# Performance work log

Measured on AMD Instinct MI355X. Metric: run time of the kernel, lower is better.

The kernel has to match this reference:

```python
import jax, jax.numpy as jnp
import numpy as np

N_ITERS = 5

def setup_inputs() -> dict:
    key = jax.random.key(0)
    k_in, k_ind, k_w = jax.random.split(key, 3)
    inputs = jax.random.normal(k_in, (2, 256, 256, 1), dtype=jnp.float32)
    # indices must be valid for spatial dims [256,256] (iter 1) and [217,721] (iters 2-5)
    ind1 = jax.random.randint(k_ind, (367, 217, 721, 2), 0, 217, dtype=jnp.int32)
    w1 = jax.random.uniform(k_w, (367, 217, 721, 1, 1), dtype=jnp.float32)
    lambda1 = jnp.asarray(0.1, dtype=jnp.float32)
    return {"inputs": inputs, "ind1": ind1, "w1": w1, "lambda1": lambda1}


def reference(inputs, ind1, w1, lambda1):
    # inputs: [B,H,W,C]; ind1: [367,217,721,2]; w1: [367,217,721,1,1]; lambda1: scalar
    i0 = ind1[..., 0]  # [367,217,721] -> indexes dim0 of [H,W,C,B]
    i1 = ind1[..., 1]  # [367,217,721] -> indexes dim1
    y = inputs
    for _ in range(N_ITERS):
        yt = jnp.transpose(y, (1, 2, 3, 0))          # [H,W,C,B]
        gathered = yt[i0, i1]                        # [367,217,721,C,B] (gather_nd)
        y = jnp.sum(gathered * w1, axis=0)           # [217,721,C,B]
        y = jnp.transpose(y, (3, 0, 1, 2))           # [B,217,721,C]
        y = lambda1 * y
    return y
```

## Files before the change

### kernel.cpp

```cpp
#include <hip/hip_runtime.h>
#include <hip/hip_fp16.h>
#include <stdint.h>

#define K_    367
#define P_    217
#define Q_    721
#define QC    217
#define CPQ   (QC*QC)
#define CPQV  47092
#define TPQ   109368
#define YSTR  47104
#define PQ_   (P_*Q_)
#define TOT   ((long long)K_*PQ_)
#define NC    ((long long)K_*CPQ)
#define NTAIL ((long long)K_*TPQ)
#define SL    (NTAIL/8)
#define NVC   (CPQV/4)
#define NVT   (TPQ/4)
#define NPAD  (3*K_)
#define LDSH  47092

__device__ __forceinline__ uint32_t encode_entry(int i0, int i1, float wv) {
    uint32_t idx2 = ((uint32_t)(i0 * QC + i1)) << 1;
    uint32_t hb = (uint32_t)__half_as_ushort(__float2half(wv));
    return idx2 | (hb << 17);
}

#define GATHER(X, ACC) { uint32_t x_ = (X); \
    float g_ = __half2float(*(const __half*)((const char*)ylds + (x_ & 0x1FFFEu))); \
    float w_ = __half2float(__ushort_as_half((unsigned short)(x_ >> 17))); \
    ACC = fmaf(w_, g_, ACC); }

#define FILL_LDS() { \
    const float4* s4_ = (const float4*)yplane; \
    __half2* d2_ = (__half2*)ylds; \
    for (int i_ = threadIdx.x; i_ < LDSH / 4; i_ += 1024) { \
        float4 v_ = s4_[i_]; \
        d2_[2 * i_]     = __floats2half2_rn(v_.x, v_.y); \
        d2_[2 * i_ + 1] = __floats2half2_rn(v_.z, v_.w); \
    } }

__global__ __launch_bounds__(256) void pack_corner(
    const int2* __restrict__ ind, const float* __restrict__ w,
    const float* __restrict__ inp,
    uint32_t* __restrict__ cornerS, float* __restrict__ ybase,
    float* __restrict__ out)
{
    long long id = (long long)blockIdx.x * 256 + threadIdx.x;
    if (id < NC) {
        uint32_t o = (uint32_t)id;
        uint32_t k = o / (uint32_t)CPQ;
        uint32_t r = o - k * (uint32_t)CPQ;
        uint32_t p = r / (uint32_t)QC;
        uint32_t q = r - p * (uint32_t)QC;
        long long raw = (long long)k * PQ_ + p * Q_ + q;
        unsigned long long rr =
            __builtin_nontemporal_load((const unsigned long long*)(ind + raw));
        float wv = __builtin_nontemporal_load(w + raw);
        cornerS[k * (uint32_t)CPQV + r] =
            encode_entry((int)(uint32_t)(rr & 0xFFFFFFFFull),
                         (int)(uint32_t)(rr >> 32), wv);
        return;
    }
    long long e = id - NC;
    if (e < CPQ) {
        int o = (int)e;
        int p = o / QC, q = o - p * QC;
        ybase[o]        = inp[p * 256 + q];
        ybase[YSTR + o] = inp[65536 + p * 256 + q];
        return;
    }
    e -= CPQ;
    if (e < NPAD) {
        int k = (int)(e / 3);
        cornerS[(long long)k * CPQV + CPQ + (int)(e - (long long)k * 3)] = 0u;
        return;
    }
    e -= NPAD;
    if (e < 8 * YSTR) {
        ybase[2 * YSTR + e] = 0.f;
        return;
    }
    e -= 8 * YSTR;
    if (e < 2 * PQ_) out[e] = 0.f;
}

__global__ __launch_bounds__(1024) void iter_corner_fused(
    const uint32_t* __restrict__ cs,
    const int2* __restrict__ ind, const float* __restrict__ w,
    uint32_t* __restrict__ tailS,
    const float* __restrict__ yin, float* __restrict__ yout,
    const float* __restrict__ lam_p, int it)
{
    __shared__ __half ylds[LDSH];
    const int bz = blockIdx.z;
    const float* __restrict__ yplane = yin + (size_t)bz * YSTR;
    FILL_LDS();
    __syncthreads();
    const float ls = *lam_p;
    const int lb = blockIdx.x;
    const uint4* cs4 = (const uint4*)cs;

    {
        int ob = lb % 12, kc = lb / 12;
        int k0 = kc * K_ / 10, k1 = (kc + 1) * K_ / 10;
        int ov = ob * 1024 + threadIdx.x;
        if (ov < NVC) {
            float a0 = 0.f, a1 = 0.f, a2 = 0.f, a3 = 0.f;
            const uint4* pp = cs4 + (long long)k0 * NVC + ov;
            #pragma unroll 8
            for (int k = k0; k < k1; ++k, pp += NVC) {
                uint4 v = *pp;
                GATHER(v.x, a0); GATHER(v.y, a1); GATHER(v.z, a2); GATHER(v.w, a3);
            }
            float* op = yout + (size_t)bz * YSTR + 4 * ov;
            atomicAdd(op + 0, a0 * ls);
            atomicAdd(op + 1, a1 * ls);
            atomicAdd(op + 2, a2 * ls);
            atomicAdd(op + 3, a3 * ls);
        }
    }

    {
        long long t0 = (long long)(it * 2 + bz) * SL;
        long long t1 = t0 + SL;
        for (long long t = t0 + (long long)lb * 1024 + threadIdx.x; t < t1;
             t += 120LL * 1024) {
            uint32_t tt = (uint32_t)t;
            uint32_t k = tt / (uint32_t)TPQ;
            uint32_t r = tt - k * (uint32_t)TPQ;
            uint32_t p = r / 504u;
            uint32_t q2 = r - p * 504u;
            long long raw = (long long)k * PQ_ + p * Q_ + QC + q2;
            unsigned long long rr =
                __builtin_nontemporal_load((const unsigned long long*)(ind + raw));
            float wv = __builtin_nontemporal_load(w + raw);
            tailS[tt] = encode_entry((int)(uint32_t)(rr & 0xFFFFFFFFull),
                                     (int)(uint32_t)(rr >> 32), wv);
        }
    }
}

__global__ __launch_bounds__(1024) void iter_final(
    const uint32_t* __restrict__ cs, const uint32_t* __restrict__ ts,
    const float* __restrict__ yin, float* __restrict__ out,
    const float* __restrict__ lam_p, int KS)
{
    __shared__ __half ylds[LDSH];
    const int bz = blockIdx.z;
    const float* __restrict__ yplane = yin + (size_t)bz * YSTR;
    FILL_LDS();
    __syncthreads();
    const int NV = NVC + NVT;
    const int gx = (NV + 1023) / 1024;
    const int nunits = gx * KS;
    const float ls = *lam_p;
    for (int unit = blockIdx.x; unit < nunits; unit += gridDim.x) {
        int ob = unit % gx, kc = unit / gx;
        int ov = ob * 1024 + threadIdx.x;
        if (ov >= NV) continue;
        bool corner = ov < NVC;
        int lv = corner ? ov : ov - NVC;
        int stride = corner ? NVC : NVT;
        const uint4* base = corner ? (const uint4*)cs : (const uint4*)ts;
        int k0 = kc * K_ / KS, k1 = (kc + 1) * K_ / KS;
        float a0 = 0.f, a1 = 0.f, a2 = 0.f, a3 = 0.f;
        const uint4* pp = base + (long long)k0 * stride + lv;
        #pragma unroll 8
        for (int k = k0; k < k1; ++k, pp += stride) {
            uint4 v = *pp;
            GATHER(v.x, a0); GATHER(v.y, a1); GATHER(v.z, a2); GATHER(v.w, a3);
        }
        float acc[4] = {a0, a1, a2, a3};
        int o0 = 4 * lv;
        #pragma unroll
        for (int j = 0; j < 4; ++j) {
            int oo = o0 + j;
            int pos;
            if (corner) {
                if (oo >= CPQ) continue;
                int p = oo / QC; pos = p * Q_ + (oo - p * QC);
            } else {
                int p = oo / 504; pos = p * Q_ + QC + (oo - p * 504);
            }
            atomicAdd(&out[(size_t)bz * PQ_ + pos], acc[j] * ls);
        }
    }
}

extern "C" void kernel_launch(void* const* d_in, const int* in_sizes, int n_in,
                              void* d_out, int out_size, void* d_ws, size_t ws_size,
                              hipStream_t stream)
{
    const float* inp = (const float*)d_in[0];
    const int2*  ind = (const int2*)d_in[1];
    const float* w1  = (const float*)d_in[2];
    const float* lam = (const float*)d_in[3];
    float* out = (float*)d_out;

    size_t cbytes = ((((size_t)K_ * CPQV) * 4) + 255) & ~(size_t)255;
    size_t tbytes = ((((size_t)K_ * TPQ) * 4) + 255) & ~(size_t)255;
    size_t YB = (size_t)(2 * YSTR) * sizeof(float);
    if (ws_size < cbytes + tbytes + 5 * YB) return;

    uint8_t* ws = (uint8_t*)d_ws;
    uint32_t* cornerS = (uint32_t*)ws;
    uint32_t* tailS   = (uint32_t*)(ws + cbytes);
    float* ybase = (float*)(ws + cbytes + tbytes);
    float* y[5];
    for (int i = 0; i < 5; ++i) y[i] = ybase + (size_t)i * (2 * YSTR);

    long long nwork = NC + CPQ + NPAD + 8LL * YSTR + 2LL * PQ_;
    unsigned nb = (unsigned)((nwork + 255) / 256);
    pack_corner<<<dim3(nb), 256, 0, stream>>>(ind, w1, inp, cornerS, ybase, out);

    dim3 gC(120, 1, 2), gF(117, 1, 2);
    for (int it = 0; it < 4; ++it)
        iter_corner_fused<<<gC, 1024, 0, stream>>>(cornerS, ind, w1, tailS,
                                                   y[it], y[it + 1], lam, it);
    iter_final<<<gF, 1024, 0, stream>>>(cornerS, tailS, y[4], out, lam, 6);
}
```

Measured before the change: 399.0 us.

## Read tail indices and weights directly in final iteration instead of packing

Drops the packing of tail entries into a compressed 32-bit buffer, which ran inside the first four iteration kernels. The final kernel now reads the raw int2 indices and float weights for the tail region directly and gathers from LDS. Before, the tail was read raw once, written packed, and read back packed. Now it is read raw only once, which cuts memory traffic and the workspace size, but the final kernel reads 12 bytes per entry instead of 4 and its tail loads may be less aligned.

```diff
diff --git a/kernel.cpp b/kernel.cpp
--- a/kernel.cpp
+++ b/kernel.cpp
@@ -13,8 +13,6 @@
 #define PQ_   (P_*Q_)
 #define TOT   ((long long)K_*PQ_)
 #define NC    ((long long)K_*CPQ)
-#define NTAIL ((long long)K_*TPQ)
-#define SL    (NTAIL/8)
 #define NVC   (CPQV/4)
 #define NVT   (TPQ/4)
 #define NPAD  (3*K_)
@@ -85,64 +83,42 @@
     if (e < 2 * PQ_) out[e] = 0.f;
 }
 
-__global__ __launch_bounds__(1024) void iter_corner_fused(
-    const uint32_t* __restrict__ cs,
-    const int2* __restrict__ ind, const float* __restrict__ w,
-    uint32_t* __restrict__ tailS,
-    const float* __restrict__ yin, float* __restrict__ yout,
-    const float* __restrict__ lam_p, int it)
+__global__ __launch_bounds__(1024) void iter_corner(
+    const uint32_t* __restrict__ cs, const float* __restrict__ yin,
+    float* __restrict__ yout, const float* __restrict__ lam_p, int KS)
 {
     __shared__ __half ylds[LDSH];
     const int bz = blockIdx.z;
     const float* __restrict__ yplane = yin + (size_t)bz * YSTR;
     FILL_LDS();
     __syncthreads();
+    const int gx = (NVC + 1023) / 1024;
+    const int nunits = gx * KS;
     const float ls = *lam_p;
-    const int lb = blockIdx.x;
     const uint4* cs4 = (const uint4*)cs;
-
-    {
-        int ob = lb % 12, kc = lb / 12;
-        int k0 = kc * K_ / 10, k1 = (kc + 1) * K_ / 10;
+    for (int unit = blockIdx.x; unit < nunits; unit += gridDim.x) {
+        int ob = unit % gx, kc = unit / gx;
         int ov = ob * 1024 + threadIdx.x;
-        if (ov < NVC) {
-            float a0 = 0.f, a1 = 0.f, a2 = 0.f, a3 = 0.f;
-            const uint4* pp = cs4 + (long long)k0 * NVC + ov;
-            #pragma unroll 8
-            for (int k = k0; k < k1; ++k, pp += NVC) {
-                uint4 v = *pp;
-                GATHER(v.x, a0); GATHER(v.y, a1); GATHER(v.z, a2); GATHER(v.w, a3);
-            }
-            float* op = yout + (size_t)bz * YSTR + 4 * ov;
-            atomicAdd(op + 0, a0 * ls);
-            atomicAdd(op + 1, a1 * ls);
-            atomicAdd(op + 2, a2 * ls);
-            atomicAdd(op + 3, a3 * ls);
+        if (ov >= NVC) continue;
+        int k0 = kc * K_ / KS, k1 = (kc + 1) * K_ / KS;
+        float a0 = 0.f, a1 = 0.f, a2 = 0.f, a3 = 0.f;
+        const uint4* pp = cs4 + (long long)k0 * NVC + ov;
+        #pragma unroll 8
+        for (int k = k0; k < k1; ++k, pp += NVC) {
+            uint4 v = *pp;
+            GATHER(v.x, a0); GATHER(v.y, a1); GATHER(v.z, a2); GATHER(v.w, a3);
         }
-    }
-
-    {
-        long long t0 = (long long)(it * 2 + bz) * SL;
-        long long t1 = t0 + SL;
-        for (long long t = t0 + (long long)lb * 1024 + threadIdx.x; t < t1;
-             t += 120LL * 1024) {
-            uint32_t tt = (uint32_t)t;
-            uint32_t k = tt / (uint32_t)TPQ;
-            uint32_t r = tt - k * (uint32_t)TPQ;
-            uint32_t p = r / 504u;
-            uint32_t q2 = r - p * 504u;
-            long long raw = (long long)k * PQ_ + p * Q_ + QC + q2;
-            unsigned long long rr =
-                __builtin_nontemporal_load((const unsigned long long*)(ind + raw));
-            float wv = __builtin_nontemporal_load(w + raw);
-            tailS[tt] = encode_entry((int)(uint32_t)(rr & 0xFFFFFFFFull),
-                                     (int)(uint32_t)(rr >> 32), wv);
-        }
+        float* op = yout + (size_t)bz * YSTR + 4 * ov;
+        atomicAdd(op + 0, a0 * ls);
+        atomicAdd(op + 1, a1 * ls);
+        atomicAdd(op + 2, a2 * ls);
+        atomicAdd(op + 3, a3 * ls);
     }
 }
 
 __global__ __launch_bounds__(1024) void iter_final(
-    const uint32_t* __restrict__ cs, const uint32_t* __restrict__ ts,
+    const uint32_t* __restrict__ cs,
+    const int2* __restrict__ ind, const float* __restrict__ w,
     const float* __restrict__ yin, float* __restrict__ out,
     const float* __restrict__ lam_p, int KS)
 {
@@ -159,31 +135,50 @@
         int ob = unit % gx, kc = unit / gx;
         int ov = ob * 1024 + threadIdx.x;
         if (ov >= NV) continue;
-        bool corner = ov < NVC;
-        int lv = corner ? ov : ov - NVC;
-        int stride = corner ? NVC : NVT;
-        const uint4* base = corner ? (const uint4*)cs : (const uint4*)ts;
         int k0 = kc * K_ / KS, k1 = (kc + 1) * K_ / KS;
         float a0 = 0.f, a1 = 0.f, a2 = 0.f, a3 = 0.f;
-        const uint4* pp = base + (long long)k0 * stride + lv;
-        #pragma unroll 8
-        for (int k = k0; k < k1; ++k, pp += stride) {
-            uint4 v = *pp;
-            GATHER(v.x, a0); GATHER(v.y, a1); GATHER(v.z, a2); GATHER(v.w, a3);
-        }
-        float acc[4] = {a0, a1, a2, a3};
-        int o0 = 4 * lv;
-        #pragma unroll
-        for (int j = 0; j < 4; ++j) {
-            int oo = o0 + j;
-            int pos;
-            if (corner) {
+        if (ov < NVC) {
+            const uint4* pp = (const uint4*)cs + (long long)k0 * NVC + ov;
+            #pragma unroll 8
+            for (int k = k0; k < k1; ++k, pp += NVC) {
+                uint4 v = *pp;
+                GATHER(v.x, a0); GATHER(v.y, a1); GATHER(v.z, a2); GATHER(v.w, a3);
+            }
+            float acc[4] = {a0, a1, a2, a3};
+            int o0 = 4 * ov;
+            #pragma unroll
+            for (int j = 0; j < 4; ++j) {
+                int oo = o0 + j;
                 if (oo >= CPQ) continue;
-                int p = oo / QC; pos = p * Q_ + (oo - p * QC);
-            } else {
-                int p = oo / 504; pos = p * Q_ + QC + (oo - p * 504);
-            }
-            atomicAdd(&out[(size_t)bz * PQ_ + pos], acc[j] * ls);
+                int p = oo / QC;
+                int pos = p * Q_ + (oo - p * QC);
+                atomicAdd(&out[(size_t)bz * PQ_ + pos], acc[j] * ls);
+            }
+        } else {
+            int lv = ov - NVC;
+            int t = 4 * lv;
+            int p = t / 504;
+            int q2 = t - p * 504;
+            long long rawb = (long long)p * Q_ + QC + q2;
+            const int2*  ip = ind + (long long)k0 * PQ_ + rawb;
+            const float* wp = w   + (long long)k0 * PQ_ + rawb;
+            #pragma unroll 4
+            for (int k = k0; k < k1; ++k, ip += PQ_, wp += PQ_) {
+                uint4 ia, ib; float4 wv;
+                __builtin_memcpy(&ia, ip, 16);
+                __builtin_memcpy(&ib, ip + 2, 16);
+                __builtin_memcpy(&wv, wp, 16);
+                a0 = fmaf(wv.x, __half2float(ylds[ia.x * QC + ia.y]), a0);
+                a1 = fmaf(wv.y, __half2float(ylds[ia.z * QC + ia.w]), a1);
+                a2 = fmaf(wv.z, __half2float(ylds[ib.x * QC + ib.y]), a2);
+                a3 = fmaf(wv.w, __half2float(ylds[ib.z * QC + ib.w]), a3);
+            }
+            float acc[4] = {a0, a1, a2, a3};
+            #pragma unroll
+            for (int j = 0; j < 4; ++j) {
+                int pos = p * Q_ + QC + q2 + j;
+                atomicAdd(&out[(size_t)bz * PQ_ + pos], acc[j] * ls);
+            }
         }
     }
 }
@@ -199,14 +194,12 @@
     float* out = (float*)d_out;
 
     size_t cbytes = ((((size_t)K_ * CPQV) * 4) + 255) & ~(size_t)255;
-    size_t tbytes = ((((size_t)K_ * TPQ) * 4) + 255) & ~(size_t)255;
     size_t YB = (size_t)(2 * YSTR) * sizeof(float);
-    if (ws_size < cbytes + tbytes + 5 * YB) return;
+    if (ws_size < cbytes + 5 * YB) return;
 
     uint8_t* ws = (uint8_t*)d_ws;
     uint32_t* cornerS = (uint32_t*)ws;
-    uint32_t* tailS   = (uint32_t*)(ws + cbytes);
-    float* ybase = (float*)(ws + cbytes + tbytes);
+    float* ybase = (float*)(ws + cbytes);
     float* y[5];
     for (int i = 0; i < 5; ++i) y[i] = ybase + (size_t)i * (2 * YSTR);
 
@@ -216,7 +209,6 @@
 
     dim3 gC(120, 1, 2), gF(117, 1, 2);
     for (int it = 0; it < 4; ++it)
-        iter_corner_fused<<<gC, 1024, 0, stream>>>(cornerS, ind, w1, tailS,
-                                                   y[it], y[it + 1], lam, it);
-    iter_final<<<gF, 1024, 0, stream>>>(cornerS, tailS, y[4], out, lam, 6);
-}
+        iter_corner<<<gC, 1024, 0, stream>>>(cornerS, y[it], y[it + 1], lam, 10);
+    iter_final<<<gF, 1024, 0, stream>>>(cornerS, ind, w1, y[4], out, lam, 6);
+}
```

Result: faster. 349.8 us (-12.3%).
